# Performance work log

Hardware: AMD Instinct MI355X
Metric: run time of the kernel (lower is better)

## Reference

```python
import jax, jax.numpy as jnp
import numpy as np

N = 100000   # nodes
E = 1600000  # edges (avg degree 16)
D = 128      # feature dim
L = 2        # nr_layers


def setup_inputs() -> dict:
    key = jax.random.key(0)
    k0, k1, k2, k3, k4 = jax.random.split(key, 5)
    x = jax.random.normal(k0, (N, D), dtype=jnp.float32)
    edge_index = jax.random.randint(k1, (2, E), 0, N, dtype=jnp.int32)
    edge_weight = jax.random.uniform(k2, (E,), dtype=jnp.float32)
    scale = 1.0 / np.sqrt(D)
    W_self = jax.random.normal(k3, (L, D, D), dtype=jnp.float32) * scale
    W_neigh = jax.random.normal(k4, (L, D, D), dtype=jnp.float32) * scale
    bias = jnp.zeros((L, D), dtype=jnp.float32)
    return {"x": x, "edge_index": edge_index, "edge_weight": edge_weight,
            "W_self": W_self, "W_neigh": W_neigh, "bias": bias}


def reference(x, edge_index, edge_weight, W_self, W_neigh, bias):
    src, dst = edge_index[0], edge_index[1]
    n = x.shape[0]
    # mean-aggregation denominator: number of incoming edges per node
    deg = jax.ops.segment_sum(jnp.ones_like(edge_weight), dst, num_segments=n)
    deg = jnp.maximum(deg, 1.0)[:, None]  # [N,1]
    nl = W_self.shape[0]
    for l in range(nl):
        msg = edge_weight[:, None] * x[src]                       # [E,D] gather
        agg = jax.ops.segment_sum(msg, dst, num_segments=n) / deg  # [N,D] scatter
        x = agg @ W_neigh[l] + x @ W_self[l] + bias[l]
        x = jax.nn.relu(x) if l < nl - 1 else jax.nn.sigmoid(x)
    return x
```

## Files before the change

kernel.cpp:

```cpp
#include <hip/hip_runtime.h>
#include <math.h>


#define D 128
#define BK_SHIFT 9
#define BK_NODES 512
#define CAP 10240
#define CH1 4096

typedef unsigned int uint;
typedef unsigned short ushort;
typedef __attribute__((ext_vector_type(2))) _Float16 h2;
typedef __attribute__((ext_vector_type(8))) _Float16 half8;
typedef __attribute__((ext_vector_type(4))) float f32x4;

__device__ __forceinline__ uint pkrtz(float lo, float hi) {
    auto v = __builtin_amdgcn_cvt_pkrtz(lo, hi);
    union { decltype(v) h; uint u; } c;
    c.h = v;
    return c.u;
}
__device__ __forceinline__ ushort f2h(float f) {
    return (ushort)(pkrtz(f, f) & 0xffffu);
}
__device__ __forceinline__ h2 u2h(uint u) {
    union { uint u; h2 h; } c;
    c.u = u;
    return c.h;
}
__device__ __forceinline__ uint h2u(h2 h) {
    union { h2 h; uint u; } c;
    c.h = h;
    return c.u;
}

__global__ __launch_bounds__(256) void k_prep(
    const float* __restrict__ x, uint* __restrict__ xh, int n8,
    const float* __restrict__ Wn, const float* __restrict__ Ws,
    ushort* __restrict__ wt, int wtotal,
    const int* __restrict__ src, const int* __restrict__ dst,
    const float* __restrict__ w, int E,
    int* __restrict__ bcur, int2* __restrict__ bedge,
    int nbConv, int nbW)
{
    __shared__ int h[256];
    __shared__ int gbase[256];
    const int t = threadIdx.x;
    const int bid = blockIdx.x;

    if (bid < nbConv) {
        int i = bid * 256 + t;
        if (i >= n8) return;
        const float4* p = reinterpret_cast<const float4*>(x + (size_t)i * 8);
        float4 a = p[0], b = p[1];
        uint4 o;
        o.x = pkrtz(a.x, a.y);
        o.y = pkrtz(a.z, a.w);
        o.z = pkrtz(b.x, b.y);
        o.w = pkrtz(b.z, b.w);
        reinterpret_cast<uint4*>(xh)[i] = o;
        return;
    }
    if (bid < nbConv + nbW) {
        int idx = (bid - nbConv) * 256 + t;
        if (idx >= wtotal) return;
        int l = idx >> 15;
        int j = (idx >> 8) & 127;
        int k = idx & 255;
        float v = (k < 128) ? Wn[(size_t)l * 16384 + (size_t)k * 128 + j]
                            : Ws[(size_t)l * 16384 + (size_t)(k - 128) * 128 + j];
        wt[idx] = f2h(v);
        return;
    }

    h[t] = 0;
    __syncthreads();
    const int base0 = (bid - nbConv - nbW) * CH1;
    uint pk[16]; float wr[16]; int br[16];
#pragma unroll
    for (int j = 0; j < 16; ++j) {
        int i = base0 + j * 256 + t;
        br[j] = -1;
        if (i < E) {
            int d = dst[i];
            int b = d >> BK_SHIFT;
            int r = atomicAdd(&h[b], 1);
            pk[j] = (uint)src[i] | ((uint)(d & (BK_NODES - 1)) << 17);
            wr[j] = w[i];
            br[j] = (b << 16) | r;
        }
    }
    __syncthreads();
    if (h[t] > 0) gbase[t] = atomicAdd(&bcur[t], h[t]);
    __syncthreads();
#pragma unroll
    for (int j = 0; j < 16; ++j) {
        if (br[j] >= 0) {
            int b = br[j] >> 16, r = br[j] & 0xffff;
            int slot = gbase[b] + r;
            if (slot < CAP)
                bedge[(size_t)b * CAP + slot] = make_int2((int)pk[j], __float_as_int(wr[j]));
        }
    }
}

__global__ __launch_bounds__(512) void k_sort2(
    const int2* __restrict__ bedge, const int* __restrict__ bcnt,
    int N, int2* __restrict__ rsdeg, int2* __restrict__ srcw)
{
    __shared__ int h[512];
    __shared__ int sa[512];
    __shared__ int sb[512];
    __shared__ int cur[512];
    const int t = threadIdx.x;
    const int b = blockIdx.x;
    const int gb = b * CAP;
    int cnt = bcnt[b];
    if (cnt > CAP) cnt = CAP;
    const int lo = b << BK_SHIFT;
    h[t] = 0;
    __syncthreads();
    for (int i = t; i < cnt; i += 512) {
        atomicAdd(&h[((uint)bedge[gb + i].x >> 17) & 511], 1);
    }
    __syncthreads();
    sa[t] = h[t];
    __syncthreads();
    int* sin = sa; int* sout = sb;
    for (int off = 1; off < 512; off <<= 1) {
        int v = sin[t];
        if (t >= off) v += sin[t - off];
        sout[t] = v;
        __syncthreads();
        int* tmp = sin; sin = sout; sout = tmp;
    }
    const int ex = sin[t] - h[t];
    cur[t] = ex;
    if (lo + t < N) rsdeg[lo + t] = make_int2(gb + ex, h[t]);
    __syncthreads();
    for (int i = t; i < cnt; i += 512) {
        int2 pe = bedge[gb + i];
        int n9 = ((uint)pe.x >> 17) & 511;
        int off = atomicAdd(&cur[n9], 1);
        float wv = __int_as_float(pe.y);
        srcw[gb + off] = make_int2((pe.x & 0x1FFFF) << 8, (int)pkrtz(wv, wv));
    }
}

__global__ __launch_bounds__(256, 8) void k_agg(
    const uint* __restrict__ xh,
    const int2* __restrict__ srcw,
    const int2* __restrict__ rsdeg,
    uint* __restrict__ agg, int N)
{
    const int tid = threadIdx.x;
    const int wv = tid >> 6;
    const int lane = tid & 63;
    const int node = blockIdx.x * 4 + wv;
    if (node >= N) return;
    const int q = lane >> 4;
    const int c16 = lane & 15;
    const int2 rd = rsdeg[node];
    const int st = rd.x;
    const int num = rd.y;
    const int en = st + num;

    h2 a2[4];
#pragma unroll
    for (int j = 0; j < 4; ++j) a2[j] = u2h(0u);

#pragma unroll 4
    for (int e = st + q; e < en; e += 4) {
        const int2 sw = srcw[e];
        const h2 w2 = u2h((uint)sw.y);
        const uint4 v = *reinterpret_cast<const uint4*>(
            (const char*)xh + (uint)sw.x + (c16 << 4));
        a2[0] = __builtin_elementwise_fma(w2, u2h(v.x), a2[0]);
        a2[1] = __builtin_elementwise_fma(w2, u2h(v.y), a2[1]);
        a2[2] = __builtin_elementwise_fma(w2, u2h(v.z), a2[2]);
        a2[3] = __builtin_elementwise_fma(w2, u2h(v.w), a2[3]);
    }

#pragma unroll
    for (int j = 0; j < 4; ++j) {
        a2[j] = a2[j] + u2h(__shfl_xor(h2u(a2[j]), 16));
        a2[j] = a2[j] + u2h(__shfl_xor(h2u(a2[j]), 32));
    }

    if (q == 0) {
        const float invd = 1.0f / (float)(num > 1 ? num : 1);
        const h2 iv = u2h(pkrtz(invd, invd));
        uint4 o;
        o.x = h2u(a2[0] * iv);
        o.y = h2u(a2[1] * iv);
        o.z = h2u(a2[2] * iv);
        o.w = h2u(a2[3] * iv);
        reinterpret_cast<uint4*>(agg + (size_t)node * 64)[c16] = o;
    }
}

template <int ACT, int OUTB>
__global__ __launch_bounds__(256) void k_gemm_mfma(
    const uint* __restrict__ aggh, const uint* __restrict__ xh,
    const uint* __restrict__ wt,
    const float* __restrict__ bias, void* __restrict__ xout, int N)
{
    const int tid = threadIdx.x;
    const int lane = tid & 63;
    const int wv = tid >> 6;
    const int wm = wv >> 1, wn = wv & 1;
    const int l16 = lane & 15;
    const int lq = lane >> 4;
    const int rowbase = blockIdx.x * 64 + wm * 32;
    const int colbase = wn * 64;

    half8 afrag[2][8];
#pragma unroll
    for (int mt = 0; mt < 2; ++mt) {
        int row = rowbase + mt * 16 + l16;
        if (row >= N) row = N - 1;
        const uint* arow = aggh + (size_t)row * 64;
        const uint* xrow = xh + (size_t)row * 64;
#pragma unroll
        for (int kk = 0; kk < 8; ++kk) {
            const uint* srcrow = (kk < 4) ? arow : xrow;
            uint4 u = *reinterpret_cast<const uint4*>(srcrow + (kk & 3) * 16 + lq * 4);
            afrag[mt][kk] = *reinterpret_cast<half8*>(&u);
        }
    }

#pragma unroll
    for (int nt = 0; nt < 4; ++nt) {
        const int col = colbase + nt * 16 + l16;
        const uint* wrow = wt + (size_t)col * 128;
        f32x4 acc0 = {0.f, 0.f, 0.f, 0.f};
        f32x4 acc1 = {0.f, 0.f, 0.f, 0.f};
#pragma unroll
        for (int kk = 0; kk < 8; ++kk) {
            uint4 u = *reinterpret_cast<const uint4*>(wrow + kk * 16 + lq * 4);
            half8 bfrag = *reinterpret_cast<half8*>(&u);
            acc0 = __builtin_amdgcn_mfma_f32_16x16x32_f16(afrag[0][kk], bfrag, acc0, 0, 0, 0);
            acc1 = __builtin_amdgcn_mfma_f32_16x16x32_f16(afrag[1][kk], bfrag, acc1, 0, 0, 0);
        }
        const float bv = bias[col];
#pragma unroll
        for (int mt = 0; mt < 2; ++mt) {
            const f32x4 acc = mt ? acc1 : acc0;
#pragma unroll
            for (int r = 0; r < 4; ++r) {
                int row = rowbase + mt * 16 + lq * 4 + r;
                if (row < N) {
                    float v = acc[r] + bv;
                    if (ACT == 0) v = fmaxf(v, 0.f);
                    else          v = 1.f / (1.f + __expf(-v));
                    if (OUTB) ((ushort*)xout)[(size_t)row * D + col] = f2h(v);
                    else      ((float*)xout)[(size_t)row * D + col] = v;
                }
            }
        }
    }
}

extern "C" void kernel_launch(void* const* d_in, const int* in_sizes, int n_in,
                              void* d_out, int out_size, void* d_ws, size_t ws_size,
                              hipStream_t stream) {
    const float* x      = (const float*)d_in[0];
    const int*   ei     = (const int*)d_in[1];
    const float* ew     = (const float*)d_in[2];
    const float* W_self = (const float*)d_in[3];
    const float* W_neigh= (const float*)d_in[4];
    const float* bias   = (const float*)d_in[5];
    float* out = (float*)d_out;

    const int N = in_sizes[0] / D;
    const int E = in_sizes[2];
    const int L = in_sizes[5] / D;
    const int B = (N + BK_NODES - 1) >> BK_SHIFT;

    const int* src = ei;
    const int* dst = ei + E;

    char* p = (char*)d_ws;
    auto carve = [&](size_t bytes) -> void* {
        void* r = (void*)p;
        p += (bytes + 255) & ~(size_t)255;
        return r;
    };
    int*   bcur   = (int*)carve(256 * 4);
    int2*  bedge  = (int2*)carve((size_t)B * CAP * 8);
    int2*  srcw   = (int2*)carve((size_t)B * CAP * 8);
    int2*  rsdeg  = (int2*)carve((size_t)N * 8);
    uint*  xh     = (uint*)carve((size_t)N * (D / 2) * 4);
    uint*  aggh   = (uint*)carve((size_t)N * (D / 2) * 4);
    uint*  hb     = (uint*)carve((size_t)N * (D / 2) * 4);
    uint*  wtbl   = (uint*)carve((size_t)L * 128 * 128 * 4);

    (void)hipMemsetAsync(bcur, 0, 256 * 4, stream);
    const int n8 = N * D / 8;
    const int wtotal = L * 32768;
    const int nbConv = (n8 + 255) / 256;
    const int nbW = (wtotal + 255) / 256;
    const int nbSort = (E + CH1 - 1) / CH1;
    k_prep<<<nbConv + nbW + nbSort, 256, 0, stream>>>(
        x, xh, n8, W_neigh, W_self, (ushort*)wtbl, wtotal,
        src, dst, ew, E, bcur, bedge, nbConv, nbW);
    k_sort2<<<B, 512, 0, stream>>>(bedge, bcur, N, rsdeg, srcw);

    const int nblk_agg  = (N + 3) / 4;
    const int nblk_gemm = (N + 63) / 64;
    const uint* cur = xh;
    for (int l = 0; l < L; ++l) {
        const uint* wtl = wtbl + (size_t)l * 128 * 128;
        const float* bl = bias + (size_t)l * D;

        k_agg<<<nblk_agg, 256, 0, stream>>>(cur, srcw, rsdeg, aggh, N);
        if (l < L - 1) {
            k_gemm_mfma<0, 1><<<nblk_gemm, 256, 0, stream>>>(aggh, cur, wtl, bl, hb, N);
            cur = hb;
        } else {
            k_gemm_mfma<1, 0><<<nblk_gemm, 256, 0, stream>>>(aggh, cur, wtl, bl, out, N);
        }
    }
}
```

Baseline: 264.1 us.

## Widen per-lane row loads in aggregation and reorder prep blocks, halving sort chunk

In the aggregation kernel each lane now covers 32 bytes of a source row using two 16-byte loads, so 8 lanes span a row and 8 edges are processed at once per wavefront. This adds one more shuffle-reduction stage. The prep kernel now puts the edge-bucketing blocks first, ahead of the conversion and weight blocks, and halves the edge chunk per block so there are twice as many smaller sort blocks. The intent is more memory-level parallelism on the gather and a better-balanced prep launch, at the cost of more partial accumulators to reduce and more global atomics on the bucket counters.

New measurement: 259.8 us. About the same (-1.7%).

```diff
diff --git a/kernel.cpp b/kernel.cpp
--- a/kernel.cpp
+++ b/kernel.cpp
@@ -6,7 +6,7 @@
 #define BK_SHIFT 9
 #define BK_NODES 512
 #define CAP 10240
-#define CH1 4096
+#define CH1 2048
 
 typedef unsigned int uint;
 typedef unsigned short ushort;
@@ -41,44 +41,45 @@
     const int* __restrict__ src, const int* __restrict__ dst,
     const float* __restrict__ w, int E,
     int* __restrict__ bcur, int2* __restrict__ bedge,
-    int nbConv, int nbW)
+    int nbSort, int nbConv)
 {
     __shared__ int h[256];
     __shared__ int gbase[256];
     const int t = threadIdx.x;
     const int bid = blockIdx.x;
 
-    if (bid < nbConv) {
-        int i = bid * 256 + t;
-        if (i >= n8) return;
-        const float4* p = reinterpret_cast<const float4*>(x + (size_t)i * 8);
-        float4 a = p[0], b = p[1];
-        uint4 o;
-        o.x = pkrtz(a.x, a.y);
-        o.y = pkrtz(a.z, a.w);
-        o.z = pkrtz(b.x, b.y);
-        o.w = pkrtz(b.z, b.w);
-        reinterpret_cast<uint4*>(xh)[i] = o;
+    if (bid >= nbSort) {
+        int cb = bid - nbSort;
+        if (cb < nbConv) {
+            int i = cb * 256 + t;
+            if (i >= n8) return;
+            const float4* p = reinterpret_cast<const float4*>(x + (size_t)i * 8);
+            float4 a = p[0], b = p[1];
+            uint4 o;
+            o.x = pkrtz(a.x, a.y);
+            o.y = pkrtz(a.z, a.w);
+            o.z = pkrtz(b.x, b.y);
+            o.w = pkrtz(b.z, b.w);
+            reinterpret_cast<uint4*>(xh)[i] = o;
+        } else {
+            int idx = (cb - nbConv) * 256 + t;
+            if (idx >= wtotal) return;
+            int l = idx >> 15;
+            int j = (idx >> 8) & 127;
+            int k = idx & 255;
+            float v = (k < 128) ? Wn[(size_t)l * 16384 + (size_t)k * 128 + j]
+                                : Ws[(size_t)l * 16384 + (size_t)(k - 128) * 128 + j];
+            wt[idx] = f2h(v);
+        }
         return;
     }
-    if (bid < nbConv + nbW) {
-        int idx = (bid - nbConv) * 256 + t;
-        if (idx >= wtotal) return;
-        int l = idx >> 15;
-        int j = (idx >> 8) & 127;
-        int k = idx & 255;
-        float v = (k < 128) ? Wn[(size_t)l * 16384 + (size_t)k * 128 + j]
-                            : Ws[(size_t)l * 16384 + (size_t)(k - 128) * 128 + j];
-        wt[idx] = f2h(v);
-        return;
-    }
 
     h[t] = 0;
     __syncthreads();
-    const int base0 = (bid - nbConv - nbW) * CH1;
-    uint pk[16]; float wr[16]; int br[16];
-#pragma unroll
-    for (int j = 0; j < 16; ++j) {
+    const int base0 = bid * CH1;
+    uint pk[8]; float wr[8]; int br[8];
+#pragma unroll
+    for (int j = 0; j < 8; ++j) {
         int i = base0 + j * 256 + t;
         br[j] = -1;
         if (i < E) {
@@ -94,7 +95,7 @@
     if (h[t] > 0) gbase[t] = atomicAdd(&bcur[t], h[t]);
     __syncthreads();
 #pragma unroll
-    for (int j = 0; j < 16; ++j) {
+    for (int j = 0; j < 8; ++j) {
         if (br[j] >= 0) {
             int b = br[j] >> 16, r = br[j] & 0xffff;
             int slot = gbase[b] + r;
@@ -158,31 +159,37 @@
     const int lane = tid & 63;
     const int node = blockIdx.x * 4 + wv;
     if (node >= N) return;
-    const int q = lane >> 4;
-    const int c16 = lane & 15;
+    const int q = lane >> 3;
+    const int c8 = lane & 7;
     const int2 rd = rsdeg[node];
     const int st = rd.x;
     const int num = rd.y;
     const int en = st + num;
 
-    h2 a2[4];
-#pragma unroll
-    for (int j = 0; j < 4; ++j) a2[j] = u2h(0u);
-
-#pragma unroll 4
-    for (int e = st + q; e < en; e += 4) {
+    h2 a2[8];
+#pragma unroll
+    for (int j = 0; j < 8; ++j) a2[j] = u2h(0u);
+
+#pragma unroll 2
+    for (int e = st + q; e < en; e += 8) {
         const int2 sw = srcw[e];
         const h2 w2 = u2h((uint)sw.y);
-        const uint4 v = *reinterpret_cast<const uint4*>(
-            (const char*)xh + (uint)sw.x + (c16 << 4));
-        a2[0] = __builtin_elementwise_fma(w2, u2h(v.x), a2[0]);
-        a2[1] = __builtin_elementwise_fma(w2, u2h(v.y), a2[1]);
-        a2[2] = __builtin_elementwise_fma(w2, u2h(v.z), a2[2]);
-        a2[3] = __builtin_elementwise_fma(w2, u2h(v.w), a2[3]);
-    }
-
-#pragma unroll
-    for (int j = 0; j < 4; ++j) {
+        const char* rowp = (const char*)xh + (uint)sw.x + (c8 << 5);
+        const uint4 v0 = *reinterpret_cast<const uint4*>(rowp);
+        const uint4 v1 = *reinterpret_cast<const uint4*>(rowp + 16);
+        a2[0] = __builtin_elementwise_fma(w2, u2h(v0.x), a2[0]);
+        a2[1] = __builtin_elementwise_fma(w2, u2h(v0.y), a2[1]);
+        a2[2] = __builtin_elementwise_fma(w2, u2h(v0.z), a2[2]);
+        a2[3] = __builtin_elementwise_fma(w2, u2h(v0.w), a2[3]);
+        a2[4] = __builtin_elementwise_fma(w2, u2h(v1.x), a2[4]);
+        a2[5] = __builtin_elementwise_fma(w2, u2h(v1.y), a2[5]);
+        a2[6] = __builtin_elementwise_fma(w2, u2h(v1.z), a2[6]);
+        a2[7] = __builtin_elementwise_fma(w2, u2h(v1.w), a2[7]);
+    }
+
+#pragma unroll
+    for (int j = 0; j < 8; ++j) {
+        a2[j] = a2[j] + u2h(__shfl_xor(h2u(a2[j]), 8));
         a2[j] = a2[j] + u2h(__shfl_xor(h2u(a2[j]), 16));
         a2[j] = a2[j] + u2h(__shfl_xor(h2u(a2[j]), 32));
     }
@@ -190,12 +197,18 @@
     if (q == 0) {
         const float invd = 1.0f / (float)(num > 1 ? num : 1);
         const h2 iv = u2h(pkrtz(invd, invd));
-        uint4 o;
-        o.x = h2u(a2[0] * iv);
-        o.y = h2u(a2[1] * iv);
-        o.z = h2u(a2[2] * iv);
-        o.w = h2u(a2[3] * iv);
-        reinterpret_cast<uint4*>(agg + (size_t)node * 64)[c16] = o;
+        uint4 o0, o1;
+        o0.x = h2u(a2[0] * iv);
+        o0.y = h2u(a2[1] * iv);
+        o0.z = h2u(a2[2] * iv);
+        o0.w = h2u(a2[3] * iv);
+        o1.x = h2u(a2[4] * iv);
+        o1.y = h2u(a2[5] * iv);
+        o1.z = h2u(a2[6] * iv);
+        o1.w = h2u(a2[7] * iv);
+        uint* ar = agg + (size_t)node * 64 + c8 * 8;
+        *reinterpret_cast<uint4*>(ar) = o0;
+        *reinterpret_cast<uint4*>(ar + 4) = o1;
     }
 }
 
@@ -298,12 +311,12 @@
     (void)hipMemsetAsync(bcur, 0, 256 * 4, stream);
     const int n8 = N * D / 8;
     const int wtotal = L * 32768;
+    const int nbSort = (E + CH1 - 1) / CH1;
     const int nbConv = (n8 + 255) / 256;
     const int nbW = (wtotal + 255) / 256;
-    const int nbSort = (E + CH1 - 1) / CH1;
-    k_prep<<<nbConv + nbW + nbSort, 256, 0, stream>>>(
+    k_prep<<<nbSort + nbConv + nbW, 256, 0, stream>>>(
         x, xh, n8, W_neigh, W_self, (ushort*)wtbl, wtotal,
-        src, dst, ew, E, bcur, bedge, nbConv, nbW);
+        src, dst, ew, E, bcur, bedge, nbSort, nbConv);
     k_sort2<<<B, 512, 0, stream>>>(bedge, bcur, N, rsdeg, srcw);
 
     const int nblk_agg  = (N + 3) / 4;
```
